# Performance work log

Measured on AMD Instinct MI355X. Metric: run time of the kernel, lower is better.

## Reference

```python
import jax, jax.numpy as jnp
import numpy as np

N = 50000
E = 800000
EPS = 1e-5


def setup_inputs() -> dict:
    key = jax.random.key(0)
    ks = jax.random.split(key, 8)
    x = jax.random.normal(ks[0], (N, 64), dtype=jnp.float32)
    edge_index = jax.random.randint(ks[1], (2, E), 0, N, dtype=jnp.int64)
    # Glorot-ish scaled weights
    W_rel0 = jax.random.normal(ks[2], (64, 128), dtype=jnp.float32) * (1.0 / np.sqrt(64))
    W_root0 = jax.random.normal(ks[3], (64, 128), dtype=jnp.float32) * (1.0 / np.sqrt(64))
    W_rel1 = jax.random.normal(ks[4], (128, 128), dtype=jnp.float32) * (1.0 / np.sqrt(128))
    W_root1 = jax.random.normal(ks[5], (128, 128), dtype=jnp.float32) * (1.0 / np.sqrt(128))
    return {
        "x": x,
        "edge_index": edge_index,
        "W_rel0": W_rel0,
        "b_rel0": jnp.zeros((128,), jnp.float32),
        "W_root0": W_root0,
        "gamma0": jnp.ones((128,), jnp.float32),
        "beta0": jnp.zeros((128,), jnp.float32),
        "W_rel1": W_rel1,
        "b_rel1": jnp.zeros((128,), jnp.float32),
        "W_root1": W_root1,
        "gamma1": jnp.ones((128,), jnp.float32),
        "beta1": jnp.zeros((128,), jnp.float32),
    }


def _graph_conv(x, src, dst, W_rel, b_rel, W_root):
    # aggr_out[i] = sum_{(s,i) in edges} x[s]   (PyG GraphConv, aggr='add')
    agg = jax.ops.segment_sum(x[src], dst, num_segments=N)  # [N, F_in]
    return agg @ W_rel + b_rel + x @ W_root                  # [N, F_out]


def _batchnorm(h, gamma, beta):
    mean = jnp.mean(h, axis=0)
    var = jnp.var(h, axis=0)
    return (h - mean) * jax.lax.rsqrt(var + EPS) * gamma + beta


def reference(x, edge_index, W_rel0, b_rel0, W_root0, gamma0, beta0,
              W_rel1, b_rel1, W_root1, gamma1, beta1):
    src, dst = edge_index[0], edge_index[1]
    # layer 0: conv -> BN -> ReLU (dropout p=0 is identity)
    h = _graph_conv(x, src, dst, W_rel0, b_rel0, W_root0)
    h = jax.nn.relu(_batchnorm(h, gamma0, beta0))
    # layer 1 (last): conv -> BN, no activation
    h = _graph_conv(h, src, dst, W_rel1, b_rel1, W_root1)
    h = _batchnorm(h, gamma1, beta1)
    return h
```

## Files before the change

### kernel.cpp

```cpp
#include <hip/hip_runtime.h>

#define NN 50000
#define NE 800000
#define EPSV 1e-5f

typedef unsigned int u32;
typedef short s16x8 __attribute__((ext_vector_type(8)));
typedef float f32x4 __attribute__((ext_vector_type(4)));

#define WS_NEEDED ((size_t)(NN * 64 + NN * 32 + 1024 + NN + NN + NE + 2 * 400000) * 4)

__global__ void k_fallback(float* __restrict__ out) {
  int i = blockIdx.x * 256 + threadIdx.x;
  if (i < NN * 128) out[i] = 2.0f;
}

__global__ void k_detect(const int* __restrict__ ei, int* __restrict__ mode) {
  if (threadIdx.x == 0) {
    int all0 = 1;
    for (int i = 1; i < 64; i += 2) all0 &= (ei[i] == 0);
    *mode = all0;
  }
}

__device__ __forceinline__ void load_edge(const int* __restrict__ ei, int m, int e,
                                          int& src, int& dst) {
  if (m) { src = ei[e << 1]; dst = ei[(NE + e) << 1]; }
  else   { src = ei[e];      dst = ei[NE + e]; }
  src = min(max(src, 0), NN - 1);
  dst = min(max(dst, 0), NN - 1);
}

__global__ __launch_bounds__(256) void k_hist(
    const int* __restrict__ ei, const int* __restrict__ mode,
    int* __restrict__ deg, int* __restrict__ rank) {
  int e = blockIdx.x * 256 + threadIdx.x;
  int src, dst;
  load_edge(ei, *mode, e, src, dst);
  rank[e] = atomicAdd(&deg[dst], 1);
}

__global__ __launch_bounds__(256) void k_scan1(
    const int* __restrict__ deg, int* __restrict__ bsum) {
  const int b = blockIdx.x, t = threadIdx.x;
  const int lane = t & 63, wave = t >> 6;
  int idx = b * 256 + t;
  int v = (idx < NN) ? deg[idx] : 0;
  for (int off = 32; off > 0; off >>= 1) v += __shfl_down(v, off);
  __shared__ int wt[4];
  if (lane == 0) wt[wave] = v;
  __syncthreads();
  if (t == 0) bsum[b] = wt[0] + wt[1] + wt[2] + wt[3];
}

__global__ __launch_bounds__(256) void k_scan3(
    const int* __restrict__ deg, const int* __restrict__ bsum, int* __restrict__ cur) {
  const int b = blockIdx.x, t = threadIdx.x;
  const int lane = t & 63, wave = t >> 6;
  __shared__ int wt[4];
  __shared__ int boff;
  int pv = (t < b) ? bsum[t] : 0;
  int r = pv;
  for (int off = 32; off > 0; off >>= 1) r += __shfl_down(r, off);
  if (lane == 0) wt[wave] = r;
  __syncthreads();
  if (t == 0) boff = wt[0] + wt[1] + wt[2] + wt[3];
  __syncthreads();
  int idx = b * 256 + t;
  int v = (idx < NN) ? deg[idx] : 0;
  int incl = v;
  for (int off = 1; off < 64; off <<= 1) {
    int u = __shfl_up(incl, off);
    if (lane >= off) incl += u;
  }
  if (lane == 63) wt[wave] = incl;
  __syncthreads();
  int woff = 0;
  for (int w = 0; w < wave; ++w) woff += wt[w];
  if (idx < NN) cur[idx] = boff + woff + incl - v;
}

__global__ __launch_bounds__(256) void k_place(
    const int* __restrict__ ei, const int* __restrict__ mode,
    const int* __restrict__ cur, const int* __restrict__ rank,
    int* __restrict__ csr) {
  int e = blockIdx.x * 256 + threadIdx.x;
  int src, dst;
  load_edge(ei, *mode, e, src, dst);
  csr[cur[dst] + rank[e]] = src;
}

__device__ __forceinline__ u32 pack_bf16(float lo, float hi) {
  union { float f; u32 u; } a, b;
  a.f = lo; b.f = hi;
  u32 ua = a.u + 0x7fffu + ((a.u >> 16) & 1u);
  u32 ub = b.u + 0x7fffu + ((b.u >> 16) & 1u);
  return (ua >> 16) | (ub & 0xffff0000u);
}
#define BFLO(u) __uint_as_float((u) << 16)
#define BFHI(u) __uint_as_float((u) & 0xffff0000u)

__global__ __launch_bounds__(256) void k_pack(
    const float* __restrict__ x, u32* __restrict__ xb) {
  int i = blockIdx.x * 256 + threadIdx.x;
  int n = i >> 5, c = i & 31;
  float2 v = *(const float2*)&x[n * 64 + c * 2];
  xb[i] = pack_bf16(v.x, v.y);
}

__global__ __launch_bounds__(256) void k_gather_xb(
    const u32* __restrict__ xb, const int* __restrict__ csr,
    const int* __restrict__ cur, const int* __restrict__ deg,
    float* __restrict__ aggx) {
  int tid = blockIdx.x * 256 + threadIdx.x;
  int n = tid >> 4, L = tid & 15;
  int i = cur[n];
  int end = i + deg[n];
  float a0 = 0.f, a1 = 0.f, a2 = 0.f, a3 = 0.f;
  float b0 = 0.f, b1 = 0.f, b2 = 0.f, b3 = 0.f;
  for (; i + 1 < end; i += 2) {
    int s0 = csr[i], s1 = csr[i + 1];
    uint2 u = *(const uint2*)&xb[s0 * 32 + 2 * L];
    uint2 w = *(const uint2*)&xb[s1 * 32 + 2 * L];
    a0 += BFLO(u.x); a1 += BFHI(u.x); a2 += BFLO(u.y); a3 += BFHI(u.y);
    b0 += BFLO(w.x); b1 += BFHI(w.x); b2 += BFLO(w.y); b3 += BFHI(w.y);
  }
  if (i < end) {
    int s0 = csr[i];
    uint2 u = *(const uint2*)&xb[s0 * 32 + 2 * L];
    a0 += BFLO(u.x); a1 += BFHI(u.x); a2 += BFLO(u.y); a3 += BFHI(u.y);
  }
  *(float4*)&aggx[n * 64 + 4 * L] =
      make_float4(a0 + b0, a1 + b1, a2 + b2, a3 + b3);
}

__global__ __launch_bounds__(256) void k_packW0(
    const float* __restrict__ Wrel, const float* __restrict__ Wroot,
    u32* __restrict__ Wpk0) {
  int t = blockIdx.x * 256 + threadIdx.x;
  int r = t & 3, lane = (t >> 2) & 63, s = (t >> 8) & 3, nt = t >> 10;
  int k = 32 * s + (lane >> 4) * 8 + 2 * r;
  int col = 16 * nt + (lane & 15);
  const float* W = (k < 64) ? &Wrel[k * 128 + col] : &Wroot[(k - 64) * 128 + col];
  Wpk0[t] = pack_bf16(W[0], W[128]);
}

__global__ __launch_bounds__(256) void k_gemm_a(
    const float* __restrict__ x, const float* __restrict__ aggx,
    const u32* __restrict__ Wpk0,
    float* __restrict__ h, float* __restrict__ psum, float* __restrict__ pssq) {
  __shared__ u32 As[8192];
  const int tid = threadIdx.x;
  const int nb = blockIdx.x * 128;
  char* AsB = (char*)As;
#pragma unroll
  for (int it = 0; it < 16; ++it) {
    int f = tid + 256 * it;
    int row = f >> 5, k4 = f & 31;
    int n = nb + row;
    const float* src = (k4 < 16) ? &aggx[n * 64 + 4 * k4] : &x[n * 64 + 4 * k4 - 64];
    float4 v = (n < NN) ? *(const float4*)src : make_float4(0.f, 0.f, 0.f, 0.f);
    uint2 p;
    p.x = pack_bf16(v.x, v.y);
    p.y = pack_bf16(v.z, v.w);
    int byte = row * 256 + k4 * 8;
    byte ^= (row & 7) << 4;
    *(uint2*)(AsB + byte) = p;
  }
  __syncthreads();
  const int lane = tid & 63;
  const int w = tid >> 6;
  const int lr = lane & 15;
  const int lg = lane >> 4;
  f32x4 zero = {0.f, 0.f, 0.f, 0.f};
  f32x4 acc[8][2];
#pragma unroll
  for (int m = 0; m < 8; ++m) {
    acc[m][0] = zero;
    acc[m][1] = zero;
  }
#pragma unroll
  for (int s = 0; s < 4; ++s) {
    s16x8 bf[2];
#pragma unroll
    for (int nt = 0; nt < 2; ++nt)
      bf[nt] = *(const s16x8*)&Wpk0[(((2 * w + nt) * 4 + s) * 64 + lane) * 4];
#pragma unroll
    for (int m = 0; m < 8; ++m) {
      int row = 16 * m + lr;
      int byte = row * 256 + 64 * s + 16 * lg;
      byte ^= (row & 7) << 4;
      s16x8 af = *(const s16x8*)(AsB + byte);
      acc[m][0] = __builtin_amdgcn_mfma_f32_16x16x32_bf16(af, bf[0], acc[m][0], 0, 0, 0);
      acc[m][1] = __builtin_amdgcn_mfma_f32_16x16x32_bf16(af, bf[1], acc[m][1], 0, 0, 0);
    }
  }
  float ps[2] = {0.f, 0.f}, qs[2] = {0.f, 0.f};
#pragma unroll
  for (int m = 0; m < 8; ++m) {
    int rowb = nb + 16 * m + 4 * lg;
#pragma unroll
    for (int nt = 0; nt < 2; ++nt) {
      int colg = 32 * w + 16 * nt + lr;
#pragma unroll
      for (int i = 0; i < 4; ++i) {
        float a = acc[m][nt][i];
        int n = rowb + i;
        if (n < NN) h[n * 128 + colg] = a;
        ps[nt] += a;
        qs[nt] += a * a;
      }
    }
  }
  __syncthreads();
  float* S = (float*)As;
  float* Q = S + 512;
#pragma unroll
  for (int nt = 0; nt < 2; ++nt) {
    int colg = 32 * w + 16 * nt + lr;
    S[lg * 128 + colg] = ps[nt];
    Q[lg * 128 + colg] = qs[nt];
  }
  __syncthreads();
  if (tid < 128) {
    float s = 0.f, q = 0.f;
#pragma unroll
    for (int g = 0; g < 4; ++g) { s += S[g * 128 + tid]; q += Q[g * 128 + tid]; }
    psum[blockIdx.x * 128 + tid] = s;
    pssq[blockIdx.x * 128 + tid] = q;
  }
}

__global__ __launch_bounds__(64) void k_bnfin(
    const float* __restrict__ psum, const float* __restrict__ pssq,
    const float* __restrict__ gamma, const float* __restrict__ beta,
    float* __restrict__ scale, float* __restrict__ shift, int P) {
  const int c = blockIdx.x;
  const int t = threadIdx.x;
  float S = 0.f, Q = 0.f;
  for (int p = t; p < P; p += 64) {
    S += psum[p * 128 + c];
    Q += pssq[p * 128 + c];
  }
  for (int off = 32; off > 0; off >>= 1) {
    S += __shfl_down(S, off);
    Q += __shfl_down(Q, off);
  }
  if (t == 0) {
    float mean = S * (1.0f / NN);
    float var = fmaxf(Q * (1.0f / NN) - mean * mean, 0.f);
    float sc = gamma[c] * rsqrtf(var + EPSV);
    scale[c] = sc;
    shift[c] = beta[c] - mean * sc;
  }
}

__global__ __launch_bounds__(256) void k_packW(
    const float* __restrict__ Wrel, const float* __restrict__ Wroot,
    u32* __restrict__ Wpk) {
  int t = blockIdx.x * 256 + threadIdx.x;
  int r = t & 3, lane = (t >> 2) & 63, s = (t >> 8) & 3, nt = t >> 10;
  int k = 32 * s + (lane >> 4) * 8 + 2 * r;
  int col = 16 * nt + (lane & 15);
  const float* W = (col < 128) ? &Wrel[k * 128 + col] : &Wroot[k * 128 + (col - 128)];
  Wpk[t] = pack_bf16(W[0], W[128]);
}

__global__ __launch_bounds__(256) void k_gemm_b(
    const u32* __restrict__ Wpk,
    const float* __restrict__ scale, const float* __restrict__ shift,
    u32* __restrict__ yb, float* __restrict__ h) {
  __shared__ u32 As[4096];
  const int tid = threadIdx.x;
  const int nb = blockIdx.x * 64;
  char* AsB = (char*)As;
#pragma unroll
  for (int it = 0; it < 8; ++it) {
    int f = tid + 256 * it;
    int row = f >> 5, k4 = f & 31;
    int n = nb + row;
    float4 v = (n < NN) ? *(const float4*)&h[n * 128 + 4 * k4]
                        : make_float4(0.f, 0.f, 0.f, 0.f);
    float4 sc = *(const float4*)&scale[4 * k4];
    float4 sh = *(const float4*)&shift[4 * k4];
    float t0 = fmaxf(v.x * sc.x + sh.x, 0.f);
    float t1 = fmaxf(v.y * sc.y + sh.y, 0.f);
    float t2 = fmaxf(v.z * sc.z + sh.z, 0.f);
    float t3 = fmaxf(v.w * sc.w + sh.w, 0.f);
    uint2 p;
    p.x = pack_bf16(t0, t1);
    p.y = pack_bf16(t2, t3);
    int byte = row * 256 + k4 * 8;
    byte ^= (row & 7) << 4;
    *(uint2*)(AsB + byte) = p;
  }
  __syncthreads();
  const int lane = tid & 63;
  const int w = tid >> 6;
  const int lr = lane & 15;
  const int lg = lane >> 4;
  f32x4 zero = {0.f, 0.f, 0.f, 0.f};
  f32x4 acc[4][4];
#pragma unroll
  for (int m = 0; m < 4; ++m)
#pragma unroll
    for (int nt = 0; nt < 4; ++nt) acc[m][nt] = zero;

#pragma unroll
  for (int s = 0; s < 4; ++s) {
    s16x8 af[4];
#pragma unroll
    for (int m = 0; m < 4; ++m) {
      int row = 16 * m + lr;
      int byte = row * 256 + 64 * s + 16 * lg;
      byte ^= (row & 7) << 4;
      af[m] = *(const s16x8*)(AsB + byte);
    }
    s16x8 bf[4];
#pragma unroll
    for (int nt = 0; nt < 4; ++nt) {
      int gnt = w * 4 + nt;
      bf[nt] = *(const s16x8*)&Wpk[((gnt * 4 + s) * 64 + lane) * 4];
    }
#pragma unroll
    for (int m = 0; m < 4; ++m)
#pragma unroll
      for (int nt = 0; nt < 4; ++nt)
        acc[m][nt] = __builtin_amdgcn_mfma_f32_16x16x32_bf16(
            af[m], bf[nt], acc[m][nt], 0, 0, 0);
  }
  if (w < 2) {
#pragma unroll
    for (int m = 0; m < 4; ++m) {
#pragma unroll
      for (int nt = 0; nt < 4; ++nt) {
        int colg = 64 * w + 16 * nt + lr;
        int rowb = nb + 16 * m + 4 * lg;
        float a0 = acc[m][nt][0], a1 = acc[m][nt][1];
        float a2 = acc[m][nt][2], a3 = acc[m][nt][3];
        float o0 = __shfl_xor(a0, 1), o1 = __shfl_xor(a1, 1);
        float o2 = __shfl_xor(a2, 1), o3 = __shfl_xor(a3, 1);
        int c2 = colg >> 1;
        u32 q0, q1;
        int i0;
        if ((lane & 1) == 0) {
      	  q0 = pack_bf16(a0, o0); q1 = pack_bf16(a1, o1); i0 = 0;
        } else {
          q0 = pack_bf16(o2, a2); q1 = pack_bf16(o3, a3); i0 = 2;
        }
        int n0 = rowb + i0, n1 = rowb + i0 + 1;
        if (n0 < NN) yb[n0 * 64 + c2] = q0;
        if (n1 < NN) yb[n1 * 64 + c2] = q1;
      }
    }
  } else {
#pragma unroll
    for (int m = 0; m < 4; ++m) {
#pragma unroll
      for (int nt = 0; nt < 4; ++nt) {
        int colg = 64 * (w - 2) + 16 * nt + lr;
        int rowb = nb + 16 * m + 4 * lg;
#pragma unroll
        for (int i = 0; i < 4; ++i) {
          int n = rowb + i;
          if (n < NN) h[n * 128 + colg] = acc[m][nt][i];
        }
      }
    }
  }
}

__global__ __launch_bounds__(256) void k_gather2(
    const u32* __restrict__ yb, const int* __restrict__ csr,
    const int* __restrict__ cur, const int* __restrict__ deg,
    float* __restrict__ h, float* __restrict__ psum, float* __restrict__ pssq) {
  int tid = blockIdx.x * 256 + threadIdx.x;
  int n = tid >> 4;
  int L = threadIdx.x & 15;
  int base = L << 2;
  int c0 = L << 3;
  int i = cur[n];
  int end = i + deg[n];
  float lo0 = 0.f, lo1 = 0.f, lo2 = 0.f, lo3 = 0.f;
  float hi0 = 0.f, hi1 = 0.f, hi2 = 0.f, hi3 = 0.f;
  float mo0 = 0.f, mo1 = 0.f, mo2 = 0.f, mo3 = 0.f;
  float ni0 = 0.f, ni1 = 0.f, ni2 = 0.f, ni3 = 0.f;
  for (; i + 1 < end; i += 2) {
    int s0 = csr[i], s1 = csr[i + 1];
    uint4 v = *(const uint4*)&yb[s0 * 64 + base];
    uint4 w = *(const uint4*)&yb[s1 * 64 + base];
    lo0 += BFLO(v.x); hi0 += BFHI(v.x);
    lo1 += BFLO(v.y); hi1 += BFHI(v.y);
    lo2 += BFLO(v.z); hi2 += BFHI(v.z);
    lo3 += BFLO(v.w); hi3 += BFHI(v.w);
    mo0 += BFLO(w.x); ni0 += BFHI(w.x);
    mo1 += BFLO(w.y); ni1 += BFHI(w.y);
    mo2 += BFLO(w.z); ni2 += BFHI(w.z);
    mo3 += BFLO(w.w); ni3 += BFHI(w.w);
  }
  if (i < end) {
    int s = csr[i];
    uint4 v = *(const uint4*)&yb[s * 64 + base];
    lo0 += BFLO(v.x); hi0 += BFHI(v.x);
    lo1 += BFLO(v.y); hi1 += BFHI(v.y);
    lo2 += BFLO(v.z); hi2 += BFHI(v.z);
    lo3 += BFLO(v.w); hi3 += BFHI(v.w);
  }
  float4 A = *(const float4*)&h[n * 128 + c0];
  float4 B = *(const float4*)&h[n * 128 + c0 + 4];
  float4 R0 = make_float4(A.x + lo0 + mo0, A.y + hi0 + ni0,
                          A.z + lo1 + mo1, A.w + hi1 + ni1);
  float4 R1 = make_float4(B.x + lo2 + mo2, B.y + hi2 + ni2,
                          B.z + lo3 + mo3, B.w + hi3 + ni3);
  *(float4*)&h[n * 128 + c0]     = R0;
  *(float4*)&h[n * 128 + c0 + 4] = R1;
  __shared__ float S[16 * 132], Q[16 * 132];
  const int nl = threadIdx.x >> 4;
  *(float4*)&S[nl * 132 + c0]     = R0;
  *(float4*)&S[nl * 132 + c0 + 4] = R1;
  *(float4*)&Q[nl * 132 + c0] =
      make_float4(R0.x * R0.x, R0.y * R0.y, R0.z * R0.z, R0.w * R0.w);
  *(float4*)&Q[nl * 132 + c0 + 4] =
      make_float4(R1.x * R1.x, R1.y * R1.y, R1.z * R1.z, R1.w * R1.w);
  __syncthreads();
  const int t = threadIdx.x;
  if (t < 128) {
    float s = 0.f, q = 0.f;
#pragma unroll
    for (int g = 0; g < 16; ++g) { s += S[g * 132 + t]; q += Q[g * 132 + t]; }
    psum[blockIdx.x * 128 + t] = s;
    pssq[blockIdx.x * 128 + t] = q;
  }
}

__global__ __launch_bounds__(256) void k_final(
    const float* __restrict__ h, const float* __restrict__ scale,
    const float* __restrict__ shift, float* __restrict__ out) {
  int tid = blockIdx.x * 256 + threadIdx.x;
  int base = tid << 2;
  int f4 = base & 127;
  float4 v = *(const float4*)&h[base];
  float4 sc = *(const float4*)&scale[f4];
  float4 sh = *(const float4*)&shift[f4];
  *(float4*)&out[base] = make_float4(v.x * sc.x + sh.x, v.y * sc.y + sh.y,
                                     v.z * sc.z + sh.z, v.w * sc.w + sh.w);
}

extern "C" void kernel_launch(void* const* d_in, const int* in_sizes, int n_in,
                              void* d_out, int out_size, void* d_ws, size_t ws_size,
                              hipStream_t stream) {
  if (ws_size < WS_NEEDED) {
    k_fallback<<<(NN * 128 + 255) / 256, 256, 0, stream>>>((float*)d_out);
    return;
  }
  const float* x      = (const float*)d_in[0];
  const int*   ei     = (const int*)d_in[1];
  const float* Wrel0  = (const float*)d_in[2];
  const float* Wroot0 = (const float*)d_in[4];
  const float* gamma0 = (const float*)d_in[5];
  const float* beta0  = (const float*)d_in[6];
  const float* Wrel1  = (const float*)d_in[7];
  const float* Wroot1 = (const float*)d_in[9];
  const float* gamma1 = (const float*)d_in[10];
  const float* beta1  = (const float*)d_in[11];

  float* aggx = (float*)d_ws;
  u32*   yb   = (u32*)d_ws;
  u32*   xb   = (u32*)(aggx + NN * 64);
  u32*   Wpk  = xb;
  u32*   Wpk0 = xb + 16384;
  float* st   = (float*)(xb + NN * 32);
  float* scale0 = st;       float* shift0 = st + 128;
  float* scale1 = st + 256; float* shift1 = st + 384;
  int* mode = (int*)(st + 512);
  int* bsum = (int*)(st + 576);
  int* deg = (int*)(st + 1024);
  int* cur = deg + NN;
  int* csr = cur + NN;
  float* psum = (float*)(csr + NE);
  float* pssq = psum + 400000;
  int* rank = (int*)psum;
  float* h = (float*)d_out;

  hipMemsetAsync(deg, 0, (size_t)NN * 4, stream);
  k_detect<<<1, 64, 0, stream>>>(ei, mode);
  k_hist<<<NE / 256, 256, 0, stream>>>(ei, mode, deg, rank);
  k_scan1<<<196, 256, 0, stream>>>(deg, bsum);
  k_scan3<<<196, 256, 0, stream>>>(deg, bsum, cur);
  k_place<<<NE / 256, 256, 0, stream>>>(ei, mode, cur, rank, csr);

  k_pack<<<(NN * 32) / 256, 256, 0, stream>>>(x, xb);
  k_gather_xb<<<(NN * 16) / 256, 256, 0, stream>>>(xb, csr, cur, deg, aggx);
  k_packW<<<64, 256, 0, stream>>>(Wrel1, Wroot1, Wpk);
  k_packW0<<<32, 256, 0, stream>>>(Wrel0, Wroot0, Wpk0);
  k_gemm_a<<<(NN + 127) / 128, 256, 0, stream>>>(x, aggx, Wpk0, h, psum, pssq);
  k_bnfin<<<128, 64, 0, stream>>>(psum, pssq, gamma0, beta0, scale0, shift0, 391);
  k_gemm_b<<<(NN + 63) / 64, 256, 0, stream>>>(Wpk, scale0, shift0, yb, h);
  k_gather2<<<(NN * 16) / 256, 256, 0, stream>>>(yb, csr, cur, deg, h, psum, pssq);
  k_bnfin<<<128, 64, 0, stream>>>(psum, pssq, gamma1, beta1, scale1, shift1, 3125);
  k_final<<<(NN * 128) / 1024, 256, 0, stream>>>(h, scale1, shift1, (float*)d_out);
}
```

Baseline: 274.3 us.

## Bin CSR scatter through shared-memory buckets and store aggregated features as bf16

Replaces the random CSR scatter kernel with a two-pass binning scheme. Edges are first grouped in shared memory by destination range into 196 global buckets, then each bucket is scattered into the CSR array, so writes stay local. The layer-0 aggregation output is also stored as packed bf16 instead of fp32, which halves its write and read traffic in the GEMM. This adds an extra kernel and workspace for the record buffers, and relies on each 4096-slot bin never overflowing, which holds by construction since bins map to CSR position ranges.

```diff
diff --git a/kernel.cpp b/kernel.cpp
--- a/kernel.cpp
+++ b/kernel.cpp
@@ -3,19 +3,24 @@
 #define NN 50000
 #define NE 800000
 #define EPSV 1e-5f
+#define NBIN 196
+#define CHUNK 2048
 
 typedef unsigned int u32;
 typedef short s16x8 __attribute__((ext_vector_type(8)));
 typedef float f32x4 __attribute__((ext_vector_type(4)));
 
-#define WS_NEEDED ((size_t)(NN * 64 + NN * 32 + 1024 + NN + NN + NE + 2 * 400000) * 4)
+#define WS_NEEDED \
+  ((size_t)(NN * 64 + NN * 32 + 1024 + NN + NN + NE + 2 * 400000 + 2 * 802816) * 4)
 
 __global__ void k_fallback(float* __restrict__ out) {
   int i = blockIdx.x * 256 + threadIdx.x;
   if (i < NN * 128) out[i] = 2.0f;
 }
 
-__global__ void k_detect(const int* __restrict__ ei, int* __restrict__ mode) {
+__global__ void k_detect(const int* __restrict__ ei, int* __restrict__ mode,
+                         int* __restrict__ binCur) {
+  for (int i = threadIdx.x; i < NBIN; i += 64) binCur[i] = 0;
   if (threadIdx.x == 0) {
     int all0 = 1;
     for (int i = 1; i < 64; i += 2) all0 &= (ei[i] == 0);
@@ -80,14 +85,79 @@
   if (idx < NN) cur[idx] = boff + woff + incl - v;
 }
 
-__global__ __launch_bounds__(256) void k_place(
+__global__ __launch_bounds__(256) void k_binA(
     const int* __restrict__ ei, const int* __restrict__ mode,
     const int* __restrict__ cur, const int* __restrict__ rank,
+    uint2* __restrict__ recs, int* __restrict__ binCur) {
+  __shared__ int hist[256];
+  __shared__ int lofs[256];
+  __shared__ int gofs[256];
+  __shared__ int wtot[4];
+  __shared__ uint2 buf[CHUNK];
+  const int t = threadIdx.x;
+  const int eb = blockIdx.x * CHUNK;
+  const int tot = min(CHUNK, NE - eb);
+  hist[t] = 0;
+  __syncthreads();
+  const int m = *mode;
+  int pos[CHUNK / 256], srcv[CHUNK / 256];
+#pragma unroll
+  for (int it = 0; it < CHUNK / 256; ++it) {
+    int e = eb + it * 256 + t;
+    if (e < NE) {
+      int s, d;
+      load_edge(ei, m, e, s, d);
+      int p = cur[d] + rank[e];
+      pos[it] = p;
+      srcv[it] = s;
+      atomicAdd(&hist[p >> 12], 1);
+    } else {
+      pos[it] = -1;
+    }
+  }
+  __syncthreads();
+  int v = hist[t];
+  const int lane = t & 63, wv = t >> 6;
+  int incl = v;
+  for (int off = 1; off < 64; off <<= 1) {
+    int u = __shfl_up(incl, off);
+    if (lane >= off) incl += u;
+  }
+  if (lane == 63) wtot[wv] = incl;
+  __syncthreads();
+  int woff = 0;
+  for (int w = 0; w < wv; ++w) woff += wtot[w];
+  lofs[t] = woff + incl - v;
+  if (v > 0) gofs[t] = atomicAdd(&binCur[t], v);
+  __syncthreads();
+  hist[t] = 0;
+  __syncthreads();
+#pragma unroll
+  for (int it = 0; it < CHUNK / 256; ++it) {
+    if (pos[it] >= 0) {
+      int b = pos[it] >> 12;
+      int o = atomicAdd(&hist[b], 1);
+      buf[lofs[b] + o] = make_uint2((u32)srcv[it], (u32)pos[it]);
+    }
+  }
+  __syncthreads();
+  for (int j = t; j < tot; j += 256) {
+    uint2 r = buf[j];
+    int b = (int)(r.y >> 12);
+    recs[(size_t)b * 4096 + gofs[b] + (j - lofs[b])] = r;
+  }
+}
+
+__global__ __launch_bounds__(256) void k_binB(
+    const uint2* __restrict__ recs, const int* __restrict__ binCur,
     int* __restrict__ csr) {
-  int e = blockIdx.x * 256 + threadIdx.x;
-  int src, dst;
-  load_edge(ei, *mode, e, src, dst);
-  csr[cur[dst] + rank[e]] = src;
+  const int b = blockIdx.x;
+  const int cnt = binCur[b];
+  const uint2* r = &recs[(size_t)b * 4096];
+  for (int j = threadIdx.x; j < cnt; j += 256) {
+    uint2 q = r[j];
+    csr[q.y] = (int)q.x;
+  }
 }
 
 __device__ __forceinline__ u32 pack_bf16(float lo, float hi) {
@@ -111,7 +181,7 @@
 __global__ __launch_bounds__(256) void k_gather_xb(
     const u32* __restrict__ xb, const int* __restrict__ csr,
     const int* __restrict__ cur, const int* __restrict__ deg,
-    float* __restrict__ aggx) {
+    u32* __restrict__ aggxb) {
   int tid = blockIdx.x * 256 + threadIdx.x;
   int n = tid >> 4, L = tid & 15;
   int i = cur[n];
@@ -130,8 +200,10 @@
     uint2 u = *(const uint2*)&xb[s0 * 32 + 2 * L];
     a0 += BFLO(u.x); a1 += BFHI(u.x); a2 += BFLO(u.y); a3 += BFHI(u.y);
   }
-  *(float4*)&aggx[n * 64 + 4 * L] =
-      make_float4(a0 + b0, a1 + b1, a2 + b2, a3 + b3);
+  uint2 o;
+  o.x = pack_bf16(a0 + b0, a1 + b1);
+  o.y = pack_bf16(a2 + b2, a3 + b3);
+  *(uint2*)&aggxb[n * 32 + 2 * L] = o;
 }
 
 __global__ __launch_bounds__(256) void k_packW0(
@@ -146,7 +218,7 @@
 }
 
 __global__ __launch_bounds__(256) void k_gemm_a(
-    const float* __restrict__ x, const float* __restrict__ aggx,
+    const float* __restrict__ x, const u32* __restrict__ aggxb,
     const u32* __restrict__ Wpk0,
     float* __restrict__ h, float* __restrict__ psum, float* __restrict__ pssq) {
   __shared__ u32 As[8192];
@@ -158,11 +230,15 @@
     int f = tid + 256 * it;
     int row = f >> 5, k4 = f & 31;
     int n = nb + row;
-    const float* src = (k4 < 16) ? &aggx[n * 64 + 4 * k4] : &x[n * 64 + 4 * k4 - 64];
-    float4 v = (n < NN) ? *(const float4*)src : make_float4(0.f, 0.f, 0.f, 0.f);
     uint2 p;
-    p.x = pack_bf16(v.x, v.y);
-    p.y = pack_bf16(v.z, v.w);
+    if (k4 < 16) {
+      p = (n < NN) ? *(const uint2*)&aggxb[n * 32 + 2 * k4] : make_uint2(0u, 0u);
+    } else {
+      float4 v = (n < NN) ? *(const float4*)&x[n * 64 + 4 * (k4 - 16)]
+                          : make_float4(0.f, 0.f, 0.f, 0.f);
+      p.x = pack_bf16(v.x, v.y);
+      p.y = pack_bf16(v.z, v.w);
+    }
     int byte = row * 256 + k4 * 8;
     byte ^= (row & 7) << 4;
     *(uint2*)(AsB + byte) = p;
@@ -344,7 +420,7 @@
         u32 q0, q1;
         int i0;
         if ((lane & 1) == 0) {
-      	  q0 = pack_bf16(a0, o0); q1 = pack_bf16(a1, o1); i0 = 0;
+          q0 = pack_bf16(a0, o0); q1 = pack_bf16(a1, o1); i0 = 0;
         } else {
           q0 = pack_bf16(o2, a2); q1 = pack_bf16(o3, a3); i0 = 2;
         }
@@ -465,6 +541,7 @@
   const float* beta1  = (const float*)d_in[11];
 
   float* aggx = (float*)d_ws;
+  u32*   aggxb = (u32*)d_ws;
   u32*   yb   = (u32*)d_ws;
   u32*   xb   = (u32*)(aggx + NN * 64);
   u32*   Wpk  = xb;
@@ -474,26 +551,29 @@
   float* scale1 = st + 256; float* shift1 = st + 384;
   int* mode = (int*)(st + 512);
   int* bsum = (int*)(st + 576);
+  int* binCur = (int*)(st + 772);
   int* deg = (int*)(st + 1024);
   int* cur = deg + NN;
   int* csr = cur + NN;
   float* psum = (float*)(csr + NE);
   float* pssq = psum + 400000;
   int* rank = (int*)psum;
+  uint2* recs = (uint2*)(pssq + 400000);
   float* h = (float*)d_out;
 
   hipMemsetAsync(deg, 0, (size_t)NN * 4, stream);
-  k_detect<<<1, 64, 0, stream>>>(ei, mode);
+  k_detect<<<1, 64, 0, stream>>>(ei, mode, binCur);
   k_hist<<<NE / 256, 256, 0, stream>>>(ei, mode, deg, rank);
   k_scan1<<<196, 256, 0, stream>>>(deg, bsum);
   k_scan3<<<196, 256, 0, stream>>>(deg, bsum, cur);
-  k_place<<<NE / 256, 256, 0, stream>>>(ei, mode, cur, rank, csr);
+  k_binA<<<(NE + CHUNK - 1) / CHUNK, 256, 0, stream>>>(ei, mode, cur, rank, recs, binCur);
+  k_binB<<<NBIN, 256, 0, stream>>>(recs, binCur, csr);
 
   k_pack<<<(NN * 32) / 256, 256, 0, stream>>>(x, xb);
-  k_gather_xb<<<(NN * 16) / 256, 256, 0, stream>>>(xb, csr, cur, deg, aggx);
+  k_gather_xb<<<(NN * 16) / 256, 256, 0, stream>>>(xb, csr, cur, deg, aggxb);
   k_packW<<<64, 256, 0, stream>>>(Wrel1, Wroot1, Wpk);
   k_packW0<<<32, 256, 0, stream>>>(Wrel0, Wroot0, Wpk0);
-  k_gemm_a<<<(NN + 127) / 128, 256, 0, stream>>>(x, aggx, Wpk0, h, psum, pssq);
+  k_gemm_a<<<(NN + 127) / 128, 256, 0, stream>>>(x, aggxb, Wpk0, h, psum, pssq);
   k_bnfin<<<128, 64, 0, stream>>>(psum, pssq, gamma0, beta0, scale0, shift0, 391);
   k_gemm_b<<<(NN + 63) / 64, 256, 0, stream>>>(Wpk, scale0, shift0, yb, h);
   k_gather2<<<(NN * 16) / 256, 256, 0, stream>>>(yb, csr, cur, deg, h, psum, pssq);
```

Result: slower. 291.9 us (+6.4%).
